# Kernel optimization log

Measured on AMD Instinct MI355X. Metric: run time of the kernel, lower is better.

## Reference

```python
import jax, jax.numpy as jnp
import numpy as np

RATIO_TH = 0.95
EPS = 1e-8


def _l2norm_rows(x):
    return x / jnp.sqrt(jnp.sum(jnp.square(x), axis=1, keepdims=True))


def setup_inputs() -> dict:
    key = jax.random.key(0)
    k1, k2 = jax.random.split(key)
    map_A = jax.random.normal(k1, (1, 256, 128, 128), dtype=jnp.float32)
    map_B = jax.random.normal(k2, (1, 256, 128, 128), dtype=jnp.float32)
    return {"map_A": map_A, "map_B": map_B}


def reference(map_A, map_B):
    # --- dense_feature_matching core: normalize, cosine sim, mutual-NN ratio test ---
    _, ch, hA, wA = map_A.shape
    _, _, hB, wB = map_B.shape
    d1 = _l2norm_rows(map_A.reshape(ch, -1).T)  # [N1, ch]
    d2 = _l2norm_rows(map_B.reshape(ch, -1).T)  # [N2, ch]
    N1 = d1.shape[0]

    sim = d1 @ d2.T  # [N1, N2] cosine similarity

    # A -> B top-2 (mnn_ratio_matcher)
    s12, nns12 = jax.lax.top_k(sim, 2)                       # [N1,2]
    dist12 = jnp.sqrt(jnp.maximum(2.0 - 2.0 * s12, 1e-12))   # sqrt(2-2*cos)
    nn12 = nns12[:, 0]
    ratio12 = dist12[:, 0] / (dist12[:, 1] + EPS)

    # B -> A top-2
    s21, nns21 = jax.lax.top_k(sim.T, 2)                     # [N2,2]
    dist21 = jnp.sqrt(jnp.maximum(2.0 - 2.0 * s21, 1e-12))
    nn21 = nns21[:, 0]
    ratio21 = dist21[:, 0] / (dist21[:, 1] + EPS)

    ids = jnp.arange(N1)
    mutual = nn21[nn12] == ids
    ratio = jnp.maximum(ratio12, ratio21[nn12])  # bidirectional ratio test
    valid = mutual & (ratio < RATIO_TH)

    # discard matches on the border of either feature map (fixed-shape mask
    # instead of torch boolean indexing, for jit compatibility)
    xA = ids % wA
    yA = ids // wA
    xB = nn12 % wB
    yB = nn12 // wB
    border = ((xA == 0) | (xA == wA - 1) | (yA == 0) | (yA == hA - 1) |
              (xB == 0) | (xB == wB - 1) | (yB == 0) | (yB == hB - 1))
    valid = valid & (~border)

    dist_out = jnp.where(valid[:, None], dist12, 0.0)  # [N1,2] masked distances
    return dist_out, nn12, valid
```

## Files before the change

kernel.cpp:

```cpp
#include <hip/hip_runtime.h>
#include <math.h>

#define NP 16384
#define CH 256
#define WDIM 128
#define EPSF 1e-8f

#define CHUNK 32
#define SPLITS 8
#define CPS (NP / SPLITS)
#define NCHUNK (CPS / CHUNK)
#define ROWS 256
#define NRT (NP / ROWS)
#define CHUNK_BYTES (CHUNK * CH * 2)
#define NCOLSLOT (NRT * 3)
#define CBSTRIDE 262

typedef short short8 __attribute__((ext_vector_type(8)));
typedef float floatx4 __attribute__((ext_vector_type(4)));

typedef __attribute__((address_space(1))) const unsigned int gu32;
typedef __attribute__((address_space(3))) unsigned int lu32;

#define NEG_INF_F __int_as_float(0xFF800000)

__global__ __launch_bounds__(256) void prep_kernel(
    const float* __restrict__ A, const float* __restrict__ B,
    float* __restrict__ AT, float* __restrict__ BT,
    unsigned short* __restrict__ Abf, unsigned short* __restrict__ Bbf)
{
    __shared__ float tile[64 * 257];
    __shared__ float rnv[64];
    const int bid = blockIdx.x;
    const float* __restrict__ src = (bid < 256) ? A : B;
    float* __restrict__ dstT = (bid < 256) ? AT : BT;
    unsigned short* __restrict__ dstb = (bid < 256) ? Abf : Bbf;
    const int pixBase = (bid & 255) * 64;
    const int t = threadIdx.x;

    for (int k = 0; k < 64 * 256; k += 256) {
        int idx = k + t;
        int p = idx & 63;
        int c = idx >> 6;
        tile[p * 257 + c] = src[(size_t)c * NP + pixBase + p];
    }
    __syncthreads();
    if (t < 64) {
        float s = 0.f;
        for (int c = 0; c < 256; ++c) { float v = tile[t * 257 + c]; s = fmaf(v, v, s); }
        rnv[t] = 1.0f / sqrtf(s);
    }
    __syncthreads();
    for (int k = 0; k < 64 * 256; k += 256) {
        int idx = k + t;
        int p = idx >> 8;
        int c = idx & 255;
        dstT[((size_t)(pixBase + p) << 8) + c] = tile[p * 257 + c] * rnv[p];
    }
    for (int k = 0; k < 64 * 128; k += 256) {
        int idx = k + t;
        int p = idx >> 7;
        int c2 = (idx & 127) * 2;
        float rn = rnv[p];
        float v0 = tile[p * 257 + c2] * rn;
        float v1 = tile[p * 257 + c2 + 1] * rn;
        unsigned u0 = __float_as_uint(v0); u0 = (u0 + 0x7fffu + ((u0 >> 16) & 1u)) >> 16;
        unsigned u1 = __float_as_uint(v1); u1 = (u1 + 0x7fffu + ((u1 >> 16) & 1u)) >> 16;
        unsigned sw = ((unsigned)(p & 7)) << 3;
        int e = ((pixBase + p) << 8) + (c2 ^ (int)sw);
        *(unsigned*)(dstb + e) = (u0 & 0xffffu) | (u1 << 16);
    }
}

__global__ __launch_bounds__(256, 2) void simk_kernel(
    const unsigned short* __restrict__ Abf, const unsigned short* __restrict__ Bbf,
    int* __restrict__ cand_row, unsigned* __restrict__ cand_col)
{
    __shared__ __align__(16) char smem[2 * CHUNK_BYTES];
    __shared__ __align__(16) float colbuf[32 * CBSTRIDE];
    __shared__ __align__(16) float2 colbuf2[2][32][9];
    const int bid = blockIdx.x;
    const int rt = bid >> 3;
    const int split = bid & 7;
    const int t = threadIdx.x;
    const int w = t >> 6;
    const int l = t & 63;
    const int l15 = l & 15, lhi = l >> 4;
    const int rowBase = rt * ROWS;
    const int colBase = split * CPS;

    short8 Bfr[4][8];
#pragma unroll
    for (int ni = 0; ni < 4; ++ni) {
        int pix = rowBase + w * 64 + ni * 16 + l15;
        const unsigned short* pr = Abf + ((size_t)pix << 8);
        int sw = (pix & 7) << 3;
#pragma unroll
        for (int kk = 0; kk < 8; ++kk) {
            int ke = kk * 32 + lhi * 8;
            Bfr[ni][kk] = *(const short8*)(pr + (ke ^ sw));
        }
    }
#pragma unroll
    for (int ni = 0; ni < 4; ++ni)
#pragma unroll
        for (int kk = 0; kk < 8; ++kk)
            asm volatile("" : "+v"(Bfr[ni][kk]));

    int aoff[8];
    {
        int cp = l15;
        int sw = (cp & 7) << 3;
#pragma unroll
        for (int kk = 0; kk < 8; ++kk) {
            int ke = kk * 32 + lhi * 8;
            aoff[kk] = (cp * 256 + (ke ^ sw)) * 2;
        }
    }

    float tv0[4], tv1[4];
#pragma unroll
    for (int ni = 0; ni < 4; ++ni) { tv0[ni] = NEG_INF_F; tv1[ni] = NEG_INF_F; }

    const char* gbase = (const char*)(Bbf + ((size_t)colBase << 8));
    const floatx4 fzero = {0.f, 0.f, 0.f, 0.f};
    floatx4 acc[2][4];

#define STAGE(CIDX, BUFSEL) do {                                              \
        const char* gsrc_ = gbase + (size_t)(CIDX) * CHUNK_BYTES;             \
        char* bdst_ = smem + (BUFSEL) * CHUNK_BYTES;                          \
        _Pragma("unroll")                                                     \
        for (int r_ = 0; r_ < 4; ++r_) {                                      \
            int off_ = w * 4096 + r_ * 1024;                                  \
            __builtin_amdgcn_global_load_lds((gu32*)(gsrc_ + off_ + l * 16),  \
                                             (lu32*)(bdst_ + off_), 16, 0, 0);\
        }                                                                     \
    } while (0)

#define MERGE2(CIDX) do {                                                     \
        if (t < 32) {                                                         \
            float b0_ = NEG_INF_F, b1_ = NEG_INF_F, b2_ = NEG_INF_F;          \
            _Pragma("unroll")                                                 \
            for (int j_ = 0; j_ < 8; ++j_) {                                  \
                float2 v_ = colbuf2[(CIDX) & 1][t][j_];                       \
                float k_ = v_.x, h_;                                          \
                h_ = fmaxf(b0_, k_); k_ = fminf(b0_, k_); b0_ = h_;           \
                h_ = fmaxf(b1_, k_); k_ = fminf(b1_, k_); b1_ = h_;           \
                b2_ = fmaxf(b2_, k_);                                         \
                k_ = v_.y;                                                    \
                h_ = fmaxf(b0_, k_); k_ = fminf(b0_, k_); b0_ = h_;           \
                h_ = fmaxf(b1_, k_); k_ = fminf(b1_, k_); b1_ = h_;           \
                b2_ = fmaxf(b2_, k_);                                         \
            }                                                                 \
            int colG_ = colBase + (CIDX) * 32 + t;                            \
            cand_col[(size_t)(rt * 3 + 0) * NP + colG_] = __float_as_uint(b0_);\
            cand_col[(size_t)(rt * 3 + 1) * NP + colG_] = __float_as_uint(b1_);\
            cand_col[(size_t)(rt * 3 + 2) * NP + colG_] = __float_as_uint(b2_);\
        }                                                                     \
    } while (0)

    STAGE(0, 0);

    for (int c = 0; c < NCHUNK; ++c) {
        __syncthreads();
        if (c + 1 < NCHUNK) STAGE(c + 1, (c + 1) & 1);
        if (c > 0) MERGE2(c - 1);

        {
            const char* buf = smem + (c & 1) * CHUNK_BYTES;
            __builtin_amdgcn_s_setprio(1);
            {
                short8 a0 = *(const short8*)(buf + aoff[0]);
                short8 a1 = *(const short8*)(buf + aoff[0] + 8192);
#pragma unroll
                for (int ni = 0; ni < 4; ++ni) {
                    acc[0][ni] = __builtin_amdgcn_mfma_f32_16x16x32_bf16(a0, Bfr[ni][0], fzero, 0, 0, 0);
                    acc[1][ni] = __builtin_amdgcn_mfma_f32_16x16x32_bf16(a1, Bfr[ni][0], fzero, 0, 0, 0);
                }
            }
#pragma unroll
            for (int kk = 1; kk < 8; ++kk) {
                short8 a0 = *(const short8*)(buf + aoff[kk]);
                short8 a1 = *(const short8*)(buf + aoff[kk] + 8192);
#pragma unroll
                for (int ni = 0; ni < 4; ++ni) {
                    acc[0][ni] = __builtin_amdgcn_mfma_f32_16x16x32_bf16(a0, Bfr[ni][kk], acc[0][ni], 0, 0, 0);
                    acc[1][ni] = __builtin_amdgcn_mfma_f32_16x16x32_bf16(a1, Bfr[ni][kk], acc[1][ni], 0, 0, 0);
                }
            }
            __builtin_amdgcn_s_setprio(0);
        }

        {
            const unsigned brb = ((unsigned)w << 6) | (unsigned)l15;
#pragma unroll
            for (int mi = 0; mi < 2; ++mi) {
#pragma unroll
                for (int reg = 0; reg < 4; ++reg) {
                    unsigned k0 = (__float_as_uint(acc[mi][0][reg]) & 0xFFFFF000u) | brb;
                    unsigned k1 = (__float_as_uint(acc[mi][1][reg]) & 0xFFFFF000u) | (brb | 16u);
                    unsigned k2 = (__float_as_uint(acc[mi][2][reg]) & 0xFFFFF000u) | (brb | 32u);
                    unsigned k3 = (__float_as_uint(acc[mi][3][reg]) & 0xFFFFF000u) | (brb | 48u);
                    float f0 = __uint_as_float(k0), f1 = __uint_as_float(k1);
                    float f2 = __uint_as_float(k2), f3 = __uint_as_float(k3);
                    float h01 = fmaxf(f0, f1), l01 = fminf(f0, f1);
                    float h23 = fmaxf(f2, f3), l23 = fminf(f2, f3);
                    float hi = fmaxf(h01, h23);
                    float lo = fmaxf(fminf(h01, h23), fmaxf(l01, l23));
                    int colL = mi * 16 + lhi * 4 + reg;
                    *(float2*)&colbuf[colL * CBSTRIDE + w * 32 + l15 * 2] = make_float2(hi, lo);
                }
            }
        }

        {
            const int cS = c << 5;
#pragma unroll
            for (int mi = 0; mi < 2; ++mi) {
#pragma unroll
                for (int reg = 0; reg < 4; ++reg) {
                    const int ib = (lhi * 4 + mi * 16 + reg) | cS;
#pragma unroll
                    for (int ni = 0; ni < 4; ++ni) {
                        int kb = (__float_as_int(acc[mi][ni][reg]) & 0xFFFFF000) | ib;
                        float fk = __int_as_float(kb);
                        float h = fmaxf(tv0[ni], fk);
                        float lo2 = fminf(tv0[ni], fk);
                        tv0[ni] = h;
                        tv1[ni] = fmaxf(tv1[ni], lo2);
                    }
                }
            }
        }

        __syncthreads();
        {
            int col = t >> 3, g = t & 7;
            float a = NEG_INF_F, b = NEG_INF_F;
#pragma unroll
            for (int k = 0; k < 16; ++k) {
                float2 v = *(const float2*)&colbuf[col * CBSTRIDE + 2 * (g + (k << 3))];
                float t0 = fmaxf(a, v.x);
                float t1 = fmaxf(fminf(a, v.x), fmaxf(b, v.y));
                a = t0; b = t1;
            }
            colbuf2[c & 1][col][g] = make_float2(a, b);
        }
    }
    __syncthreads();
    MERGE2(NCHUNK - 1);
#undef STAGE
#undef MERGE2

    int2* mrg = (int2*)colbuf;
#pragma unroll
    for (int ni = 0; ni < 4; ++ni) {
        int rloc = w * 64 + ni * 16 + l15;
        int2 p;
        p.x = __float_as_int(tv0[ni]);
        p.y = __float_as_int(tv1[ni]);
        mrg[rloc * 4 + lhi] = p;
    }
    __syncthreads();
    {
        float b0 = NEG_INF_F, b1 = NEG_INF_F;
#pragma unroll
        for (int q = 0; q < 4; ++q) {
            int2 p = mrg[t * 4 + q];
            int ks[2] = {p.x, p.y};
#pragma unroll
            for (int j = 0; j < 2; ++j) {
                float k = __int_as_float(ks[j]);
                float h = fmaxf(b0, k);
                float lo = fminf(b0, k);
                b0 = h;
                b1 = fmaxf(b1, lo);
            }
        }
        int rowG = rowBase + t;
        int* o = cand_row + (size_t)rowG * 16 + split * 2;
        o[0] = colBase + (__float_as_int(b0) & 0xFFF);
        o[1] = colBase + (__float_as_int(b1) & 0xFFF);
    }
}

__global__ __launch_bounds__(256) void mergecol_kernel(
    const unsigned* __restrict__ cand_col, int* __restrict__ col6)
{
    int col = blockIdx.x * 256 + threadIdx.x;
    float bv0 = NEG_INF_F, bv1 = NEG_INF_F, bv2 = NEG_INF_F;
    float bv3 = NEG_INF_F, bv4 = NEG_INF_F, bv5 = NEG_INF_F;
    for (int s = 0; s < NCOLSLOT; ++s) {
        float k = __uint_as_float(cand_col[(size_t)s * NP + col]);
        float h;
        h = fmaxf(bv0, k); k = fminf(bv0, k); bv0 = h;
        h = fmaxf(bv1, k); k = fminf(bv1, k); bv1 = h;
        h = fmaxf(bv2, k); k = fminf(bv2, k); bv2 = h;
        h = fmaxf(bv3, k); k = fminf(bv3, k); bv3 = h;
        h = fmaxf(bv4, k); k = fminf(bv4, k); bv4 = h;
        bv5 = fmaxf(bv5, k);
    }
    const float thr = bv5;
    int r0 = 0, r1 = 0, r2 = 0, r3 = 0, r4 = 0, r5 = 0;
    int cnt = 0;
    for (int s = 0; s < NCOLSLOT; ++s) {
        unsigned ku = cand_col[(size_t)s * NP + col];
        float k = __uint_as_float(ku);
        bool take = (k >= thr) && (cnt < 6);
        int row = (s / 3) * 256 + (int)(ku & 0xFFu);
        r0 = (take && cnt == 0) ? row : r0;
        r1 = (take && cnt == 1) ? row : r1;
        r2 = (take && cnt == 2) ? row : r2;
        r3 = (take && cnt == 3) ? row : r3;
        r4 = (take && cnt == 4) ? row : r4;
        r5 = (take && cnt == 5) ? row : r5;
        cnt += take ? 1 : 0;
    }
    int* o = col6 + (size_t)col * 6;
    o[0] = r0; o[1] = r1; o[2] = r2; o[3] = r3; o[4] = r4; o[5] = r5;
}

__global__ __launch_bounds__(256) void rescore_row_kernel(
    const float* __restrict__ AT, const float* __restrict__ BT,
    const int* __restrict__ cand_row, float4* __restrict__ final12)
{
    const int t = threadIdx.x;
    const int w = t >> 6, l = t & 63;
    const int row = blockIdx.x * 4 + w;
    float4 rv = *(const float4*)(AT + ((size_t)row << 8) + l * 4);
    float v0 = -4.f, v1 = -4.f; int i0 = 0x7fffffff, i1 = 0x7fffffff;
    const int* __restrict__ cl = cand_row + (size_t)row * 16;
#pragma unroll 4
    for (int j = 0; j < 16; ++j) {
        int idx = cl[j];
        float4 cv = *(const float4*)(BT + ((size_t)idx << 8) + l * 4);
        float d = rv.x * cv.x;
        d = fmaf(rv.y, cv.y, d);
        d = fmaf(rv.z, cv.z, d);
        d = fmaf(rv.w, cv.w, d);
#pragma unroll
        for (int m = 1; m < 64; m <<= 1) d += __shfl_xor(d, m, 64);
        if (d > v0 || (d == v0 && idx < i0)) {
            v1 = v0; i1 = i0; v0 = d; i0 = idx;
        } else if (d > v1 || (d == v1 && idx < i1)) {
            v1 = d; i1 = idx;
        }
    }
    if (l == 0) {
        float4 r; r.x = v0; r.y = v1;
        r.z = __int_as_float(i0); r.w = __int_as_float(i1);
        final12[row] = r;
    }
}

__global__ __launch_bounds__(256) void rescore_col_kernel(
    const float* __restrict__ AT, const float* __restrict__ BT,
    const int* __restrict__ col6,
    int* __restrict__ nn21, float* __restrict__ ratio21)
{
    const int t = threadIdx.x;
    const int w = t >> 6, l = t & 63;
    const int col = blockIdx.x * 4 + w;
    float4 rv = *(const float4*)(BT + ((size_t)col << 8) + l * 4);
    float v0 = -4.f, v1 = -4.f; int i0 = 0x7fffffff, i1 = 0x7fffffff;
    const int* __restrict__ cl = col6 + (size_t)col * 6;
#pragma unroll
    for (int j = 0; j < 6; ++j) {
        int idx = cl[j];
        float4 cv = *(const float4*)(AT + ((size_t)idx << 8) + l * 4);
        float d = rv.x * cv.x;
        d = fmaf(rv.y, cv.y, d);
        d = fmaf(rv.z, cv.z, d);
        d = fmaf(rv.w, cv.w, d);
#pragma unroll
        for (int m = 1; m < 64; m <<= 1) d += __shfl_xor(d, m, 64);
        if (d > v0 || (d == v0 && idx < i0)) {
            v1 = v0; i1 = i0; v0 = d; i0 = idx;
        } else if (d > v1 || (d == v1 && idx < i1)) {
            v1 = d; i1 = idx;
        }
    }
    if (l == 0) {
        nn21[col] = i0;
        float d0 = sqrtf(fmaxf(2.f - 2.f * v0, 1e-12f));
        float d1 = sqrtf(fmaxf(2.f - 2.f * v1, 1e-12f));
        ratio21[col] = d0 / (d1 + EPSF);
    }
}

__global__ void final_kernel(const float4* __restrict__ final12,
                             const int* __restrict__ nn21,
                             const float* __restrict__ ratio21,
                             float* __restrict__ out) {
    int i = blockIdx.x * blockDim.x + threadIdx.x;
    float4 a = final12[i];
    float d0 = sqrtf(fmaxf(2.f - 2.f * a.x, 1e-12f));
    float d1 = sqrtf(fmaxf(2.f - 2.f * a.y, 1e-12f));
    int nn = __float_as_int(a.z);
    float r12 = d0 / (d1 + EPSF);
    bool mutual = (nn21[nn] == i);
    float r = fmaxf(r12, ratio21[nn]);
    int xA = i & (WDIM - 1), yA = i >> 7;
    int xB = nn & (WDIM - 1), yB = nn >> 7;
    bool border = (xA == 0) || (xA == WDIM - 1) || (yA == 0) || (yA == WDIM - 1) ||
                  (xB == 0) || (xB == WDIM - 1) || (yB == 0) || (yB == WDIM - 1);
    bool valid = mutual && (r < 0.95f) && !border;
    out[2 * i]       = valid ? d0 : 0.f;
    out[2 * i + 1]   = valid ? d1 : 0.f;
    out[2 * NP + i]  = (float)nn;
    out[3 * NP + i]  = valid ? 1.f : 0.f;
}

extern "C" void kernel_launch(void* const* d_in, const int* in_sizes, int n_in,
                              void* d_out, int out_size, void* d_ws, size_t ws_size,
                              hipStream_t stream) {
    (void)in_sizes; (void)n_in; (void)out_size; (void)ws_size;
    const float* A = (const float*)d_in[0];
    const float* B = (const float*)d_in[1];
    float* out = (float*)d_out;

    char* ws = (char*)d_ws;
    float* AT = (float*)ws;
    float* BT = AT + (size_t)NP * CH;
    unsigned short* Abf = (unsigned short*)(BT + (size_t)NP * CH);
    unsigned short* Bbf = Abf + (size_t)NP * CH;
    int* cand_row = (int*)(Bbf + (size_t)NP * CH);
    unsigned* cand_col = (unsigned*)(cand_row + (size_t)NP * 16);
    int* col6 = (int*)(cand_col + (size_t)NCOLSLOT * NP);
    float4* final12 = (float4*)(col6 + (size_t)NP * 6);
    int* nn21 = (int*)(final12 + NP);
    float* ratio21 = (float*)(nn21 + NP);

    prep_kernel<<<512, 256, 0, stream>>>(A, B, AT, BT, Abf, Bbf);
    simk_kernel<<<NRT * SPLITS, 256, 0, stream>>>(Abf, Bbf, cand_row, cand_col);
    mergecol_kernel<<<NP / 256, 256, 0, stream>>>(cand_col, col6);
    rescore_row_kernel<<<NP / 4, 256, 0, stream>>>(AT, BT, cand_row, final12);
    rescore_col_kernel<<<NP / 4, 256, 0, stream>>>(AT, BT, col6, nn21, ratio21);
    final_kernel<<<NP / 256, 256, 0, stream>>>(final12, nn21, ratio21, out);
}
```

Before: 294.4 us.

## Keep top-3 per split with finer row keys and rescore only global top-8

The similarity kernel now tracks separate top-2 per MFMA sub-tile and merges them into a top-3 per column split, storing packed score|index keys with an 11-bit index mask instead of 12-bit. The row rescore kernel selects the global top-8 among the 24 candidate keys by bf16-approx score and only rescores those in fp32, instead of rescoring a fixed 16. This is meant to improve candidate recall and reduce gather/dot work in the rescore. The cost is extra registers and compares in the hot kernel plus a small sort in rescore, and approximate-key thresholding may change which candidates are checked.

```diff
diff --git a/kernel.cpp b/kernel.cpp
--- a/kernel.cpp
+++ b/kernel.cpp
@@ -23,6 +23,7 @@
 typedef __attribute__((address_space(3))) unsigned int lu32;
 
 #define NEG_INF_F __int_as_float(0xFF800000)
+#define ROWKEY_MASK 0xFFFFF800u
 
 __global__ __launch_bounds__(256) void prep_kernel(
     const float* __restrict__ A, const float* __restrict__ B,
@@ -74,7 +75,7 @@
 
 __global__ __launch_bounds__(256, 2) void simk_kernel(
     const unsigned short* __restrict__ Abf, const unsigned short* __restrict__ Bbf,
-    int* __restrict__ cand_row, unsigned* __restrict__ cand_col)
+    unsigned* __restrict__ cand_row, unsigned* __restrict__ cand_col)
 {
     __shared__ __align__(16) char smem[2 * CHUNK_BYTES];
     __shared__ __align__(16) float colbuf[32 * CBSTRIDE];
@@ -118,9 +119,11 @@
         }
     }
 
-    float tv0[4], tv1[4];
-#pragma unroll
-    for (int ni = 0; ni < 4; ++ni) { tv0[ni] = NEG_INF_F; tv1[ni] = NEG_INF_F; }
+    float tv0[2][4], tv1[2][4];
+#pragma unroll
+    for (int mi = 0; mi < 2; ++mi)
+#pragma unroll
+        for (int ni = 0; ni < 4; ++ni) { tv0[mi][ni] = NEG_INF_F; tv1[mi][ni] = NEG_INF_F; }
 
     const char* gbase = (const char*)(Bbf + ((size_t)colBase << 8));
     const floatx4 fzero = {0.f, 0.f, 0.f, 0.f};
@@ -197,10 +200,10 @@
             for (int mi = 0; mi < 2; ++mi) {
 #pragma unroll
                 for (int reg = 0; reg < 4; ++reg) {
-                    unsigned k0 = (__float_as_uint(acc[mi][0][reg]) & 0xFFFFF000u) | brb;
-                    unsigned k1 = (__float_as_uint(acc[mi][1][reg]) & 0xFFFFF000u) | (brb | 16u);
-                    unsigned k2 = (__float_as_uint(acc[mi][2][reg]) & 0xFFFFF000u) | (brb | 32u);
-                    unsigned k3 = (__float_as_uint(acc[mi][3][reg]) & 0xFFFFF000u) | (brb | 48u);
+                    unsigned k0 = (__float_as_uint(acc[mi][0][reg]) & 0xFFFFFF00u) | brb;
+                    unsigned k1 = (__float_as_uint(acc[mi][1][reg]) & 0xFFFFFF00u) | (brb | 16u);
+                    unsigned k2 = (__float_as_uint(acc[mi][2][reg]) & 0xFFFFFF00u) | (brb | 32u);
+                    unsigned k3 = (__float_as_uint(acc[mi][3][reg]) & 0xFFFFFF00u) | (brb | 48u);
                     float f0 = __uint_as_float(k0), f1 = __uint_as_float(k1);
                     float f2 = __uint_as_float(k2), f3 = __uint_as_float(k3);
                     float h01 = fmaxf(f0, f1), l01 = fminf(f0, f1);
@@ -222,12 +225,12 @@
                     const int ib = (lhi * 4 + mi * 16 + reg) | cS;
 #pragma unroll
                     for (int ni = 0; ni < 4; ++ni) {
-                        int kb = (__float_as_int(acc[mi][ni][reg]) & 0xFFFFF000) | ib;
+                        int kb = (__float_as_int(acc[mi][ni][reg]) & (int)ROWKEY_MASK) | ib;
                         float fk = __int_as_float(kb);
-                        float h = fmaxf(tv0[ni], fk);
-                        float lo2 = fminf(tv0[ni], fk);
-                        tv0[ni] = h;
-                        tv1[ni] = fmaxf(tv1[ni], lo2);
+                        float h = fmaxf(tv0[mi][ni], fk);
+                        float lo2 = fminf(tv0[mi][ni], fk);
+                        tv0[mi][ni] = h;
+                        tv1[mi][ni] = fmaxf(tv1[mi][ni], lo2);
                     }
                 }
             }
@@ -252,35 +255,37 @@
 #undef STAGE
 #undef MERGE2
 
-    int2* mrg = (int2*)colbuf;
+    int4* mrg = (int4*)colbuf;
 #pragma unroll
     for (int ni = 0; ni < 4; ++ni) {
         int rloc = w * 64 + ni * 16 + l15;
-        int2 p;
-        p.x = __float_as_int(tv0[ni]);
-        p.y = __float_as_int(tv1[ni]);
+        int4 p;
+        p.x = __float_as_int(tv0[0][ni]);
+        p.y = __float_as_int(tv1[0][ni]);
+        p.z = __float_as_int(tv0[1][ni]);
+        p.w = __float_as_int(tv1[1][ni]);
         mrg[rloc * 4 + lhi] = p;
     }
     __syncthreads();
     {
-        float b0 = NEG_INF_F, b1 = NEG_INF_F;
+        float b0 = NEG_INF_F, b1 = NEG_INF_F, b2 = NEG_INF_F;
 #pragma unroll
         for (int q = 0; q < 4; ++q) {
-            int2 p = mrg[t * 4 + q];
-            int ks[2] = {p.x, p.y};
-#pragma unroll
-            for (int j = 0; j < 2; ++j) {
-                float k = __int_as_float(ks[j]);
-                float h = fmaxf(b0, k);
-                float lo = fminf(b0, k);
-                b0 = h;
-                b1 = fmaxf(b1, lo);
+            int4 p = mrg[t * 4 + q];
+            int ks[4] = {p.x, p.y, p.z, p.w};
+#pragma unroll
+            for (int j = 0; j < 4; ++j) {
+                float k = __int_as_float(ks[j]), h;
+                h = fmaxf(b0, k); k = fminf(b0, k); b0 = h;
+                h = fmaxf(b1, k); k = fminf(b1, k); b1 = h;
+                b2 = fmaxf(b2, k);
             }
         }
         int rowG = rowBase + t;
-        int* o = cand_row + (size_t)rowG * 16 + split * 2;
-        o[0] = colBase + (__float_as_int(b0) & 0xFFF);
-        o[1] = colBase + (__float_as_int(b1) & 0xFFF);
+        unsigned* o = cand_row + (size_t)rowG * 24 + split * 3;
+        o[0] = __float_as_uint(b0);
+        o[1] = __float_as_uint(b1);
+        o[2] = __float_as_uint(b2);
     }
 }
 
@@ -322,28 +327,49 @@
 
 __global__ __launch_bounds__(256) void rescore_row_kernel(
     const float* __restrict__ AT, const float* __restrict__ BT,
-    const int* __restrict__ cand_row, float4* __restrict__ final12)
+    const unsigned* __restrict__ cand_row, float4* __restrict__ final12)
 {
     const int t = threadIdx.x;
     const int w = t >> 6, l = t & 63;
     const int row = blockIdx.x * 4 + w;
     float4 rv = *(const float4*)(AT + ((size_t)row << 8) + l * 4);
+    const unsigned* __restrict__ cl = cand_row + (size_t)row * 24;
+
+    float t8[8];
+#pragma unroll
+    for (int q = 0; q < 8; ++q) t8[q] = NEG_INF_F;
+#pragma unroll
+    for (int s = 0; s < 24; ++s) {
+        float k = __uint_as_float(cl[s]);
+#pragma unroll
+        for (int q = 0; q < 8; ++q) {
+            float h = fmaxf(t8[q], k);
+            k = fminf(t8[q], k);
+            t8[q] = h;
+        }
+    }
+    const float thr = t8[7];
+
     float v0 = -4.f, v1 = -4.f; int i0 = 0x7fffffff, i1 = 0x7fffffff;
-    const int* __restrict__ cl = cand_row + (size_t)row * 16;
-#pragma unroll 4
-    for (int j = 0; j < 16; ++j) {
-        int idx = cl[j];
-        float4 cv = *(const float4*)(BT + ((size_t)idx << 8) + l * 4);
-        float d = rv.x * cv.x;
-        d = fmaf(rv.y, cv.y, d);
-        d = fmaf(rv.z, cv.z, d);
-        d = fmaf(rv.w, cv.w, d);
-#pragma unroll
-        for (int m = 1; m < 64; m <<= 1) d += __shfl_xor(d, m, 64);
-        if (d > v0 || (d == v0 && idx < i0)) {
-            v1 = v0; i1 = i0; v0 = d; i0 = idx;
-        } else if (d > v1 || (d == v1 && idx < i1)) {
-            v1 = d; i1 = idx;
+    int taken = 0;
+    for (int s = 0; s < 24; ++s) {
+        unsigned ku = cl[s];
+        float kf = __uint_as_float(ku);
+        if (kf >= thr && taken < 8) {
+            ++taken;
+            int idx = (s / 3) * CPS + (int)(ku & 0x7FFu);
+            float4 cv = *(const float4*)(BT + ((size_t)idx << 8) + l * 4);
+            float d = rv.x * cv.x;
+            d = fmaf(rv.y, cv.y, d);
+            d = fmaf(rv.z, cv.z, d);
+            d = fmaf(rv.w, cv.w, d);
+#pragma unroll
+            for (int m = 1; m < 64; m <<= 1) d += __shfl_xor(d, m, 64);
+            if (d > v0 || (d == v0 && idx < i0)) {
+                v1 = v0; i1 = i0; v0 = d; i0 = idx;
+            } else if (d > v1 || (d == v1 && idx < i1)) {
+                v1 = d; i1 = idx;
+            }
         }
     }
     if (l == 0) {
@@ -424,8 +450,8 @@
     float* BT = AT + (size_t)NP * CH;
     unsigned short* Abf = (unsigned short*)(BT + (size_t)NP * CH);
     unsigned short* Bbf = Abf + (size_t)NP * CH;
-    int* cand_row = (int*)(Bbf + (size_t)NP * CH);
-    unsigned* cand_col = (unsigned*)(cand_row + (size_t)NP * 16);
+    unsigned* cand_row = (unsigned*)(Bbf + (size_t)NP * CH);
+    unsigned* cand_col = cand_row + (size_t)NP * 24;
     int* col6 = (int*)(cand_col + (size_t)NCOLSLOT * NP);
     float4* final12 = (float4*)(col6 + (size_t)NP * 6);
     int* nn21 = (int*)(final12 + NP);
```

After: 291.4 us. About the same (-1.0%).
